# Performance work log

Hardware: AMD Instinct MI355X
Metric: run time of the kernel (lower is better)

Reference implementation:

```python
import jax, jax.numpy as jnp
import numpy as np

EMBED_DIM = 1024
NUM_HEADS = 16
HEAD_DIM = EMBED_DIM // NUM_HEADS


def setup_inputs() -> dict:
    key = jax.random.key(0)
    ks = jax.random.split(key, 7)
    B, S, D = 2, 2048, EMBED_DIM
    s = 1.0 / np.sqrt(D)
    return {
        "x": jax.random.normal(ks[0], (B, S, D), dtype=jnp.float32),
        "Wq": jax.random.normal(ks[1], (D, D), dtype=jnp.float32) * s,
        "bq": jax.random.normal(ks[2], (D,), dtype=jnp.float32) * 0.01,
        "Wk": jax.random.normal(ks[3], (D, D), dtype=jnp.float32) * s,
        "bk": jax.random.normal(ks[4], (D,), dtype=jnp.float32) * 0.01,
        "Wv": jax.random.normal(ks[5], (D, D), dtype=jnp.float32) * s,
        "bv": jax.random.normal(ks[6], (D,), dtype=jnp.float32) * 0.01,
    }


def reference(x, Wq, bq, Wk, bk, Wv, bv):
    B, S, D = x.shape
    H, Hd = NUM_HEADS, HEAD_DIM
    # QKV projections, then split heads: [B, S, D] -> [B, H, S, Hd]
    q = (x @ Wq + bq).reshape(B, S, H, Hd).transpose(0, 2, 1, 3)
    k = (x @ Wk + bk).reshape(B, S, H, Hd).transpose(0, 2, 1, 3)
    v = (x @ Wv + bv).reshape(B, S, H, Hd).transpose(0, 2, 1, 3)
    # NOTE: the original module applies NO 1/sqrt(head_dim) scaling.
    energy = jnp.einsum("bhqd,bhkd->bhqk", q, k)  # [B, H, S, S]
    attn = jax.nn.softmax(energy, axis=-1)
    out = jnp.einsum("bhqk,bhkd->bhqd", attn, v)
    return out.transpose(0, 2, 1, 3).reshape(B, S, D)
```

## Files before the change

kernel.cpp:

```cpp
#include <hip/hip_runtime.h>
#include <stdint.h>
#include <stddef.h>

typedef _Float16 half_t;
typedef __attribute__((ext_vector_type(8))) _Float16 h16x8;
typedef __attribute__((ext_vector_type(4))) _Float16 h16x4;
typedef __attribute__((ext_vector_type(4))) float f32x4;

#define MFMA16(a, b, c) __builtin_amdgcn_mfma_f32_16x16x32_f16(a, b, c, 0, 0, 0)
#define EXP2(x) __builtin_amdgcn_exp2f(x)

#define SW(row, slot) ((((slot) ^ ((row) & 7))) * 8)

__global__ __launch_bounds__(256) void cvt_x_kernel(const float* __restrict__ x,
                                                    half_t* __restrict__ xh, int n8) {
    int i = blockIdx.x * blockDim.x + threadIdx.x;
    if (i >= n8) return;
    const float4* xv = (const float4*)x;
    float4 a = xv[i * 2 + 0];
    float4 b = xv[i * 2 + 1];
    h16x8 o;
    o[0] = (half_t)a.x; o[1] = (half_t)a.y; o[2] = (half_t)a.z; o[3] = (half_t)a.w;
    o[4] = (half_t)b.x; o[5] = (half_t)b.y; o[6] = (half_t)b.z; o[7] = (half_t)b.w;
    ((h16x8*)xh)[i] = o;
}

__global__ __launch_bounds__(256) void cvt_w_kernel(const float* __restrict__ Wq,
                                                    const float* __restrict__ Wk,
                                                    const float* __restrict__ Wv,
                                                    half_t* __restrict__ Wt) {
    __shared__ float t[32][33];
    const float* W = (blockIdx.z == 0) ? Wq : ((blockIdx.z == 1) ? Wk : Wv);
    int k0 = blockIdx.y * 32, n0 = blockIdx.x * 32;
    int tid = threadIdx.x;
    int r = tid >> 3;
    int c4 = (tid & 7) * 4;
    float4 v = *(const float4*)&W[(size_t)(k0 + r) * 1024 + n0 + c4];
    t[r][c4 + 0] = v.x; t[r][c4 + 1] = v.y; t[r][c4 + 2] = v.z; t[r][c4 + 3] = v.w;
    __syncthreads();
    half_t* o = Wt + (size_t)blockIdx.z * 1024 * 1024 + (size_t)(n0 + r) * 1024 + k0 + c4;
    h16x4 h;
    h[0] = (half_t)t[c4 + 0][r];
    h[1] = (half_t)t[c4 + 1][r];
    h[2] = (half_t)t[c4 + 2][r];
    h[3] = (half_t)t[c4 + 3][r];
    *(h16x4*)o = h;
}

__global__ __launch_bounds__(256, 2) void gemm_qkv_kernel(
    const half_t* __restrict__ xh,
    const half_t* __restrict__ Wt,
    const float* __restrict__ bq, const float* __restrict__ bk,
    const float* __restrict__ bv,
    half_t* __restrict__ qkv)
{
    const int p = blockIdx.z;
    const float* bias = (p == 0) ? bq : ((p == 1) ? bk : bv);
    const half_t* Wp = Wt + (size_t)p * 1024 * 1024;
    const int n0 = blockIdx.x * 128, m0 = blockIdx.y * 128;

    __shared__ half_t Al[128][72];
    __shared__ half_t Bl[128][72];

    const int tid = threadIdx.x;
    const int lane = tid & 63, wid = tid >> 6;
    const int wm = wid >> 1, wn = wid & 1;
    const int g = lane >> 4, r = lane & 15;

    const int srow = tid >> 3;
    const int scol = (tid & 7) * 8;

    f32x4 acc[4][4];
#pragma unroll
    for (int a = 0; a < 4; a++)
#pragma unroll
        for (int c = 0; c < 4; c++) acc[a][c] = (f32x4){0.f, 0.f, 0.f, 0.f};

    h16x8 ra[4], rb[4];
#pragma unroll
    for (int i = 0; i < 4; i++) {
        ra[i] = *(const h16x8*)&xh[(size_t)(m0 + srow + i * 32) * 1024 + scol];
        rb[i] = *(const h16x8*)&Wp[(size_t)(n0 + srow + i * 32) * 1024 + scol];
    }

    for (int k0 = 0; k0 < 1024; k0 += 64) {
        __syncthreads();
#pragma unroll
        for (int i = 0; i < 4; i++) {
            *(h16x8*)&Al[srow + i * 32][scol] = ra[i];
            *(h16x8*)&Bl[srow + i * 32][scol] = rb[i];
        }
        __syncthreads();

        int kn = (k0 + 64) & 1023;
#pragma unroll
        for (int i = 0; i < 4; i++) {
            ra[i] = *(const h16x8*)&xh[(size_t)(m0 + srow + i * 32) * 1024 + kn + scol];
            rb[i] = *(const h16x8*)&Wp[(size_t)(n0 + srow + i * 32) * 1024 + kn + scol];
        }

#pragma unroll
        for (int t = 0; t < 2; t++) {
            h16x8 af[4], bf[4];
#pragma unroll
            for (int mi = 0; mi < 4; mi++)
                af[mi] = *(const h16x8*)&Al[wm * 64 + mi * 16 + r][t * 32 + g * 8];
#pragma unroll
            for (int ni = 0; ni < 4; ni++)
                bf[ni] = *(const h16x8*)&Bl[wn * 64 + ni * 16 + r][t * 32 + g * 8];
#pragma unroll
            for (int mi = 0; mi < 4; mi++)
#pragma unroll
                for (int ni = 0; ni < 4; ni++)
                    acc[mi][ni] = MFMA16(af[mi], bf[ni], acc[mi][ni]);
        }
    }

    float bn[4];
#pragma unroll
    for (int ni = 0; ni < 4; ni++) bn[ni] = bias[n0 + wn * 64 + ni * 16 + r];

    if (p == 2) {
        half_t* outp = qkv + (size_t)2 * 4194304;
#pragma unroll
        for (int mi = 0; mi < 4; mi++) {
            int m = m0 + wm * 64 + mi * 16 + g * 4;
            int b = m >> 11, s = m & 2047;
#pragma unroll
            for (int ni = 0; ni < 4; ni++) {
                int n = n0 + wn * 64 + ni * 16 + r;
                int h = n >> 6, hd = n & 63;
                h16x4 pk;
#pragma unroll
                for (int i = 0; i < 4; i++) pk[i] = (half_t)(acc[mi][ni][i] + bn[ni]);
                *(h16x4*)&outp[((size_t)(b * 16 + h) * 64 + hd) * 2048 + s] = pk;
            }
        }
    } else {
        half_t* outp = qkv + (size_t)p * 4194304;
#pragma unroll
        for (int mi = 0; mi < 4; mi++) {
#pragma unroll
            for (int ni = 0; ni < 4; ni++) {
                int n = n0 + wn * 64 + ni * 16 + r;
                int h = n >> 6, hd = n & 63;
#pragma unroll
                for (int i = 0; i < 4; i++) {
                    int m = m0 + wm * 64 + mi * 16 + g * 4 + i;
                    int b = m >> 11, s = m & 2047;
                    float v = acc[mi][ni][i] + bn[ni];
                    outp[(((size_t)(b * 16 + h) * 2048 + s) << 6) + hd] = (half_t)v;
                }
            }
        }
    }
}

__global__ __launch_bounds__(256, 3) void attn_kernel(
    const half_t* __restrict__ Qg,
    const half_t* __restrict__ Kg,
    const half_t* __restrict__ Vtg,
    float* __restrict__ out)
{
    __shared__ half_t Kl[2][64][64];
    __shared__ half_t Vl[2][64][64];
    __shared__ half_t Pl[4][32][64];

    const int tid = threadIdx.x;
    const int lane = tid & 63, wid = tid >> 6;
    const int g = lane >> 4, r = lane & 15;
    const int bh = blockIdx.y;
    const int b = bh >> 4, h = bh & 15;
    const half_t* Qb = Qg + (size_t)bh * 131072;
    const half_t* Kb = Kg + (size_t)bh * 131072;
    const half_t* Vb = Vtg + (size_t)bh * 131072;
    const int q0 = blockIdx.x * 128 + wid * 32;

    h16x8 qf[2][2];
#pragma unroll
    for (int qg = 0; qg < 2; qg++)
#pragma unroll
        for (int t = 0; t < 2; t++) {
            qf[qg][t] = *(const h16x8*)&Qb[(size_t)(q0 + qg * 16 + r) * 64 + t * 32 + g * 8];
            qf[qg][t] *= (half_t)1.44269504f;
        }

    f32x4 o[2][4];
#pragma unroll
    for (int qg = 0; qg < 2; qg++)
#pragma unroll
        for (int d = 0; d < 4; d++) o[qg][d] = (f32x4){0.f, 0.f, 0.f, 0.f};
    float m_run[2] = {0.f, 0.f}, l_run[2] = {0.f, 0.f};

    const int srow = tid >> 3;
    const int sslot = tid & 7;
    const int sc8 = sslot * 8;

#pragma unroll
    for (int half = 0; half < 2; half++) {
        int row = srow + half * 32;
        *(h16x8*)&Kl[0][row][SW(row, sslot)] = *(const h16x8*)&Kb[row * 64 + sc8];
        *(h16x8*)&Vl[0][row][SW(row, sslot)] = *(const h16x8*)&Vb[(size_t)row * 2048 + sc8];
    }

    h16x8 kreg[2], vreg[2];
    int cur = 0;

    auto compute_tile = [&](int cb) {
        f32x4 e[2][4];
#pragma unroll
        for (int kc = 0; kc < 4; kc++) {
            e[0][kc] = (f32x4){0.f, 0.f, 0.f, 0.f};
            e[1][kc] = (f32x4){0.f, 0.f, 0.f, 0.f};
#pragma unroll
            for (int t = 0; t < 2; t++) {
                h16x8 kf = *(const h16x8*)&Kl[cb][kc * 16 + r][SW(r, t * 4 + g)];
                e[0][kc] = MFMA16(kf, qf[0][t], e[0][kc]);
                e[1][kc] = MFMA16(kf, qf[1][t], e[1][kc]);
            }
        }

#pragma unroll
        for (int qg = 0; qg < 2; qg++) {
            float t0 = fmaxf(fmaxf(e[qg][0][0], e[qg][0][1]), e[qg][0][2]);
            float t1 = fmaxf(fmaxf(e[qg][0][3], e[qg][1][0]), e[qg][1][1]);
            float t2 = fmaxf(fmaxf(e[qg][1][2], e[qg][1][3]), e[qg][2][0]);
            float t3 = fmaxf(fmaxf(e[qg][2][1], e[qg][2][2]), e[qg][2][3]);
            float t4 = fmaxf(fmaxf(e[qg][3][0], e[qg][3][1]), e[qg][3][2]);
            float tm = fmaxf(fmaxf(t0, t1), fmaxf(fmaxf(t2, t3), fmaxf(t4, e[qg][3][3])));
            tm = fmaxf(tm, __shfl_xor(tm, 16));
            tm = fmaxf(tm, __shfl_xor(tm, 32));

            float ps0 = 0.f, ps1 = 0.f, ps2 = 0.f, ps3 = 0.f;
#pragma unroll
            for (int i = 0; i < 4; i++) { e[qg][0][i] = EXP2(e[qg][0][i] - m_run[qg]); ps0 += e[qg][0][i]; }
#pragma unroll
            for (int i = 0; i < 4; i++) { e[qg][1][i] = EXP2(e[qg][1][i] - m_run[qg]); ps1 += e[qg][1][i]; }
#pragma unroll
            for (int i = 0; i < 4; i++) { e[qg][2][i] = EXP2(e[qg][2][i] - m_run[qg]); ps2 += e[qg][2][i]; }
#pragma unroll
            for (int i = 0; i < 4; i++) { e[qg][3][i] = EXP2(e[qg][3][i] - m_run[qg]); ps3 += e[qg][3][i]; }

            if (!__all(tm <= m_run[qg] + 8.f)) {
                float nm = fmaxf(m_run[qg], tm);
                float sc = EXP2(m_run[qg] - nm);
                m_run[qg] = nm;
                l_run[qg] *= sc;
#pragma unroll
                for (int kc = 0; kc < 4; kc++)
#pragma unroll
                    for (int i = 0; i < 4; i++) e[qg][kc][i] *= sc;
                ps0 *= sc; ps1 *= sc; ps2 *= sc; ps3 *= sc;
#pragma unroll
                for (int i = 0; i < 4; i++) {
                    float sci = __shfl(sc, (lane & 48) | (g * 4 + i));
#pragma unroll
                    for (int d = 0; d < 4; d++) o[qg][d][i] *= sci;
                }
            }

            float ps = (ps0 + ps1) + (ps2 + ps3);
            ps += __shfl_xor(ps, 16);
            ps += __shfl_xor(ps, 32);
            l_run[qg] += ps;

#pragma unroll
            for (int kc = 0; kc < 4; kc++) {
                h16x4 pk;
#pragma unroll
                for (int i = 0; i < 4; i++) pk[i] = (half_t)e[qg][kc][i];
                *(h16x4*)&Pl[wid][qg * 16 + r][SW(r, 2 * kc + (g >> 1)) + (g & 1) * 4] = pk;
            }
        }
        asm volatile("s_waitcnt lgkmcnt(0)" ::: "memory");
        __builtin_amdgcn_sched_barrier(0);

#pragma unroll
        for (int ks = 0; ks < 2; ks++) {
            h16x8 pf0 = *(const h16x8*)&Pl[wid][r][SW(r, ks * 4 + g)];
            h16x8 pf1 = *(const h16x8*)&Pl[wid][16 + r][SW(r, ks * 4 + g)];
#pragma unroll
            for (int d = 0; d < 4; d++) {
                h16x8 vf = *(const h16x8*)&Vl[cb][d * 16 + r][SW(r, ks * 4 + g)];
                o[0][d] = MFMA16(pf0, vf, o[0][d]);
                o[1][d] = MFMA16(pf1, vf, o[1][d]);
            }
        }
    };

    for (int kt = 0; kt < 32; ++kt) {
        int ktn = (kt + 1) & 31;
        __syncthreads();
#pragma unroll
        for (int half = 0; half < 2; half++) {
            int row = srow + half * 32;
            kreg[half] = *(const h16x8*)&Kb[ktn * 4096 + row * 64 + sc8];
            vreg[half] = *(const h16x8*)&Vb[(size_t)row * 2048 + ktn * 64 + sc8];
        }
        compute_tile(cur);
#pragma unroll
        for (int half = 0; half < 2; half++) {
            int row = srow + half * 32;
            *(h16x8*)&Kl[cur ^ 1][row][SW(row, sslot)] = kreg[half];
            *(h16x8*)&Vl[cur ^ 1][row][SW(row, sslot)] = vreg[half];
        }
        cur ^= 1;
    }

#pragma unroll
    for (int qg = 0; qg < 2; qg++)
#pragma unroll
        for (int i = 0; i < 4; i++) {
            float li = __shfl(l_run[qg], (lane & 48) | (g * 4 + i));
            float inv = 1.0f / li;
            int s = q0 + qg * 16 + g * 4 + i;
            float* op = out + (size_t)(b * 2048 + s) * 1024 + h * 64 + r;
#pragma unroll
            for (int d = 0; d < 4; d++) op[d * 16] = o[qg][d][i] * inv;
        }
}

extern "C" void kernel_launch(void* const* d_in, const int* in_sizes, int n_in,
                              void* d_out, int out_size, void* d_ws, size_t ws_size,
                              hipStream_t stream) {
    const float* x  = (const float*)d_in[0];
    const float* Wq = (const float*)d_in[1];
    const float* bq = (const float*)d_in[2];
    const float* Wk = (const float*)d_in[3];
    const float* bk = (const float*)d_in[4];
    const float* Wv = (const float*)d_in[5];
    const float* bv = (const float*)d_in[6];
    float* out = (float*)d_out;

    half_t* xh  = (half_t*)d_ws;
    half_t* Wt  = (half_t*)((char*)d_ws + (size_t)8 * 1024 * 1024);
    half_t* qkv = (half_t*)((char*)d_ws + (size_t)14 * 1024 * 1024);
    half_t* Qh  = qkv;
    half_t* Kh  = qkv + (size_t)4194304;
    half_t* Vth = qkv + (size_t)8388608;

    cvt_x_kernel<<<2048, 256, 0, stream>>>(x, xh, 524288);
    cvt_w_kernel<<<dim3(32, 32, 3), 256, 0, stream>>>(Wq, Wk, Wv, Wt);
    gemm_qkv_kernel<<<dim3(8, 32, 3), 256, 0, stream>>>(xh, Wt, bq, bk, bv, qkv);
    attn_kernel<<<dim3(16, 32), 256, 0, stream>>>(Qh, Kh, Vth, out);
}
```

Measured before the change: 109.3 us.

## Load K/V fragments directly from global into registers, drop LDS staging, remap blocks per XCD

Result: slower. 168.7 us (+54.4%).

```diff
diff --git a/kernel.cpp b/kernel.cpp
--- a/kernel.cpp
+++ b/kernel.cpp
@@ -156,25 +156,29 @@
     }
 }
 
-__global__ __launch_bounds__(256, 3) void attn_kernel(
+__global__ __launch_bounds__(256) void attn_kernel(
     const half_t* __restrict__ Qg,
     const half_t* __restrict__ Kg,
     const half_t* __restrict__ Vtg,
     float* __restrict__ out)
 {
-    __shared__ half_t Kl[2][64][64];
-    __shared__ half_t Vl[2][64][64];
     __shared__ half_t Pl[4][32][64];
 
     const int tid = threadIdx.x;
     const int lane = tid & 63, wid = tid >> 6;
     const int g = lane >> 4, r = lane & 15;
-    const int bh = blockIdx.y;
+
+    const int bid = blockIdx.x;
+    const int xcd = bid & 7;
+    const int t_  = bid >> 3;
+    const int qblk = t_ & 15;
+    const int bh = xcd + 8 * (t_ >> 4);
+
     const int b = bh >> 4, h = bh & 15;
     const half_t* Qb = Qg + (size_t)bh * 131072;
     const half_t* Kb = Kg + (size_t)bh * 131072;
     const half_t* Vb = Vtg + (size_t)bh * 131072;
-    const int q0 = blockIdx.x * 128 + wid * 32;
+    const int q0 = qblk * 128 + wid * 32;
 
     h16x8 qf[2][2];
 #pragma unroll
@@ -192,21 +196,27 @@
         for (int d = 0; d < 4; d++) o[qg][d] = (f32x4){0.f, 0.f, 0.f, 0.f};
     float m_run[2] = {0.f, 0.f}, l_run[2] = {0.f, 0.f};
 
-    const int srow = tid >> 3;
-    const int sslot = tid & 7;
-    const int sc8 = sslot * 8;
-
-#pragma unroll
-    for (int half = 0; half < 2; half++) {
-        int row = srow + half * 32;
-        *(h16x8*)&Kl[0][row][SW(row, sslot)] = *(const h16x8*)&Kb[row * 64 + sc8];
-        *(h16x8*)&Vl[0][row][SW(row, sslot)] = *(const h16x8*)&Vb[(size_t)row * 2048 + sc8];
-    }
-
-    h16x8 kreg[2], vreg[2];
-    int cur = 0;
-
-    auto compute_tile = [&](int cb) {
+    auto loadK = [&](int kt, h16x8* kf) {
+#pragma unroll
+        for (int kc = 0; kc < 4; kc++)
+#pragma unroll
+            for (int t = 0; t < 2; t++)
+                kf[kc * 2 + t] =
+                    *(const h16x8*)&Kb[(size_t)kt * 4096 + kc * 1024 + r * 64 + t * 32 + g * 8];
+    };
+    auto loadV = [&](int kt, h16x8* vf) {
+#pragma unroll
+        for (int d = 0; d < 4; d++)
+#pragma unroll
+            for (int ks = 0; ks < 2; ks++)
+                vf[d * 2 + ks] =
+                    *(const h16x8*)&Vb[(size_t)(d * 16 + r) * 2048 + kt * 64 + ks * 32 + g * 8];
+    };
+
+    h16x8 kf[8], vf[8];
+    loadK(0, kf);
+
+    for (int kt = 0; kt < 32; ++kt) {
         f32x4 e[2][4];
 #pragma unroll
         for (int kc = 0; kc < 4; kc++) {
@@ -214,11 +224,13 @@
             e[1][kc] = (f32x4){0.f, 0.f, 0.f, 0.f};
 #pragma unroll
             for (int t = 0; t < 2; t++) {
-                h16x8 kf = *(const h16x8*)&Kl[cb][kc * 16 + r][SW(r, t * 4 + g)];
-                e[0][kc] = MFMA16(kf, qf[0][t], e[0][kc]);
-                e[1][kc] = MFMA16(kf, qf[1][t], e[1][kc]);
-            }
-        }
+                e[0][kc] = MFMA16(kf[kc * 2 + t], qf[0][t], e[0][kc]);
+                e[1][kc] = MFMA16(kf[kc * 2 + t], qf[1][t], e[1][kc]);
+            }
+        }
+
+        loadV(kt, vf);
+        loadK((kt + 1) & 31, kf);
 
 #pragma unroll
         for (int qg = 0; qg < 2; qg++) {
@@ -281,30 +293,10 @@
             h16x8 pf1 = *(const h16x8*)&Pl[wid][16 + r][SW(r, ks * 4 + g)];
 #pragma unroll
             for (int d = 0; d < 4; d++) {
-                h16x8 vf = *(const h16x8*)&Vl[cb][d * 16 + r][SW(r, ks * 4 + g)];
-                o[0][d] = MFMA16(pf0, vf, o[0][d]);
-                o[1][d] = MFMA16(pf1, vf, o[1][d]);
-            }
-        }
-    };
-
-    for (int kt = 0; kt < 32; ++kt) {
-        int ktn = (kt + 1) & 31;
-        __syncthreads();
-#pragma unroll
-        for (int half = 0; half < 2; half++) {
-            int row = srow + half * 32;
-            kreg[half] = *(const h16x8*)&Kb[ktn * 4096 + row * 64 + sc8];
-            vreg[half] = *(const h16x8*)&Vb[(size_t)row * 2048 + ktn * 64 + sc8];
-        }
-        compute_tile(cur);
-#pragma unroll
-        for (int half = 0; half < 2; half++) {
-            int row = srow + half * 32;
-            *(h16x8*)&Kl[cur ^ 1][row][SW(row, sslot)] = kreg[half];
-            *(h16x8*)&Vl[cur ^ 1][row][SW(row, sslot)] = vreg[half];
-        }
-        cur ^= 1;
+                o[0][d] = MFMA16(pf0, vf[d * 2 + ks], o[0][d]);
+                o[1][d] = MFMA16(pf1, vf[d * 2 + ks], o[1][d]);
+            }
+        }
     }
 
 #pragma unroll
@@ -342,5 +334,5 @@
     cvt_x_kernel<<<2048, 256, 0, stream>>>(x, xh, 524288);
     cvt_w_kernel<<<dim3(32, 32, 3), 256, 0, stream>>>(Wq, Wk, Wv, Wt);
     gemm_qkv_kernel<<<dim3(8, 32, 3), 256, 0, stream>>>(xh, Wt, bq, bk, bv, qkv);
-    attn_kernel<<<dim3(16, 32), 256, 0, stream>>>(Qh, Kh, Vth, out);
-}
+    attn_kernel<<<512, 256, 0, stream>>>(Qh, Kh, Vth, out);
+}
```
